# Kernel tuning notes

Hardware: AMD Instinct MI355X
Metric: run time of the kernel (lower is better)

Reference implementation:

```python
import jax, jax.numpy as jnp
import numpy as np

N_HEADS = 16
N_KV_HEADS = 4
HEAD_DIM = 64
ROPE_BASE = 10000.0

def _rope_cos_sin(T, dtype):
    # flash-attn style: cos/sin of shape [T, head_dim//2]
    inv_freq = 1.0 / (ROPE_BASE ** (jnp.arange(0, HEAD_DIM, 2, dtype=jnp.float32) / HEAD_DIM))
    freqs = jnp.arange(T, dtype=jnp.float32)[:, None] * inv_freq[None, :]  # [T, D/2]
    return jnp.cos(freqs).astype(dtype), jnp.sin(freqs).astype(dtype)

def _apply_rope(x, cos, sin):
    # x: [B, H, T, D], non-interleaved rotate-half on full head dim
    d2 = HEAD_DIM // 2
    x1, x2 = x[..., :d2], x[..., d2:]
    c = cos[None, None, :, :]
    s = sin[None, None, :, :]
    return jnp.concatenate([x1 * c - x2 * s, x2 * c + x1 * s], axis=-1)

def setup_inputs() -> dict:
    key = jax.random.key(0)
    ks = jax.random.split(key, 6)
    B, T, D = 1, 4096, 1024
    def g(k, shape, scale):
        return jax.random.normal(k, shape, dtype=jnp.float32) * scale
    return {
        "query": g(ks[0], (B, T, D), 1.0),
        "Wq": g(ks[1], (D, D), D ** -0.5),
        "Wk": g(ks[2], (D, N_KV_HEADS * HEAD_DIM), D ** -0.5),
        "Wv": g(ks[3], (D, N_KV_HEADS * HEAD_DIM), D ** -0.5),
        "W1": g(ks[4], (D, 4 * D), D ** -0.5),
        "W2": g(ks[5], (4 * D, D), (4 * D) ** -0.5),
    }

def reference(query, Wq, Wk, Wv, W1, W2):
    B, T, D = query.shape
    # QKV projections -> [B, H, T, Dh]
    q = (query @ Wq).reshape(B, T, N_HEADS, HEAD_DIM).transpose(0, 2, 1, 3)
    k = (query @ Wk).reshape(B, T, N_KV_HEADS, HEAD_DIM).transpose(0, 2, 1, 3)
    v = (query @ Wv).reshape(B, T, N_KV_HEADS, HEAD_DIM).transpose(0, 2, 1, 3)
    # RoPE (seqlen_offset = 0, no cache)
    cos, sin = _rope_cos_sin(T, q.dtype)
    q = _apply_rope(q, cos, sin)
    k = _apply_rope(k, cos, sin)
    # GQA: repeat KV heads to match Q heads
    n_rep = N_HEADS // N_KV_HEADS
    k = jnp.repeat(k, n_rep, axis=1)
    v = jnp.repeat(v, n_rep, axis=1)
    # Scaled dot-product attention, causal
    scale = HEAD_DIM ** -0.5
    scores = jnp.einsum("bhqd,bhkd->bhqk", q, k) * scale
    i = jnp.arange(T)[:, None]
    j = jnp.arange(T)[None, :]
    scores = jnp.where(j > i, jnp.finfo(scores.dtype).min, scores)
    attn = jax.nn.softmax(scores, axis=-1)
    out = jnp.einsum("bhqk,bhkd->bhqd", attn, v)  # [B, H, T, Dh]
    out = out.transpose(0, 2, 1, 3).reshape(B, T, D)
    # out_proj: Linear -> SiLU -> Linear (use_swiglu=True path)
    return jax.nn.silu(out @ W1) @ W2
```

## Files before the change

kernel.cpp:

```cpp
#include <hip/hip_runtime.h>
#include <stdint.h>

typedef unsigned short u16;
typedef __bf16 bf16x8 __attribute__((ext_vector_type(8)));
typedef float f32x4 __attribute__((ext_vector_type(4)));

#define T_SEQ 4096
#define DMODEL 1024

__device__ __forceinline__ float bf2f(u16 x) {
  union { uint32_t u; float f; } v; v.u = ((uint32_t)x) << 16; return v.f;
}
__device__ __forceinline__ u16 f2bf(float f) {
  union { float f; uint32_t u; } v; v.f = f;
  return (u16)((v.u + 0x7FFFu + ((v.u >> 16) & 1u)) >> 16);
}
__device__ __forceinline__ float fexp2(float x) {
#if __has_builtin(__builtin_amdgcn_exp2f)
  return __builtin_amdgcn_exp2f(x);
#else
  return __expf(x * 0.6931471805599453f);
#endif
}
__device__ __forceinline__ uint32_t pack_bf16(float lo, float hi) {
#if __has_builtin(__builtin_amdgcn_cvt_pk_bf16_f32)
  typedef __bf16 bf16x2_t __attribute__((ext_vector_type(2)));
  union { bf16x2_t v; uint32_t u; } c;
  c.v = __builtin_amdgcn_cvt_pk_bf16_f32(lo, hi);
  return c.u;
#else
  union { float f; uint32_t u; } a, b;
  a.f = lo; b.f = hi;
  return __builtin_amdgcn_perm(b.u + 0x8000u, a.u + 0x8000u, 0x07060302u);
#endif
}
__device__ __forceinline__ void async16(void* lds, const void* g) {
  __builtin_amdgcn_global_load_lds(
      (__attribute__((address_space(1))) void*)const_cast<void*>(g),
      (__attribute__((address_space(3))) void*)lds, 16, 0, 0);
}
__device__ __forceinline__ void storeC(u16* C, size_t i, float v) { C[i] = f2bf(v); }
__device__ __forceinline__ void storeC(float* C, size_t i, float v) { C[i] = v; }

__global__ void __launch_bounds__(256) f2b_copy(const float* __restrict__ in,
                                                u16* __restrict__ out, int n) {
  int idx = (blockIdx.x * 256 + threadIdx.x) * 4;
  if (idx >= n) return;
  float4 v = *(const float4*)(in + idx);
  union { u16 s[4]; uint2 q; } b;
  b.s[0] = f2bf(v.x); b.s[1] = f2bf(v.y); b.s[2] = f2bf(v.z); b.s[3] = f2bf(v.w);
  *(uint2*)(out + idx) = b.q;
}

__global__ void __launch_bounds__(256) wtrans(const float* __restrict__ in,
                                              u16* __restrict__ out, int K, int N) {
  __shared__ float tile[64][65];
  const int n0 = blockIdx.x * 64, k0 = blockIdx.y * 64;
  const int tid = threadIdx.x;
  const int r = tid >> 2, c = (tid & 3) * 16;
#pragma unroll
  for (int j = 0; j < 4; ++j) {
    float4 v = *(const float4*)&in[(size_t)(k0 + r) * N + n0 + c + j * 4];
    tile[r][c + j * 4 + 0] = v.x; tile[r][c + j * 4 + 1] = v.y;
    tile[r][c + j * 4 + 2] = v.z; tile[r][c + j * 4 + 3] = v.w;
  }
  __syncthreads();
  union { u16 s[16]; uint4 q[2]; } buf;
#pragma unroll
  for (int j = 0; j < 16; ++j) buf.s[j] = f2bf(tile[c + j][r]);
  u16* dst = out + (size_t)(n0 + r) * K + k0 + c;
  *(uint4*)(dst) = buf.q[0];
  *(uint4*)(dst + 8) = buf.q[1];
}

__global__ void __launch_bounds__(256) vtrans(const u16* __restrict__ qkv,
                                              u16* __restrict__ Vt) {
  __shared__ u16 tile[64][65];
  const int t0 = blockIdx.x * 64, h = blockIdx.y;
  const int tid = threadIdx.x;
  const int r = tid >> 2, q4 = (tid & 3) * 16;
  const u16* src = qkv + (size_t)(t0 + r) * 1536 + 1280 + h * 64 + q4;
  union { u16 s[16]; uint4 q[2]; } buf;
  buf.q[0] = *(const uint4*)(src);
  buf.q[1] = *(const uint4*)(src + 8);
#pragma unroll
  for (int j = 0; j < 16; ++j) tile[r][q4 + j] = buf.s[j];
  __syncthreads();
#pragma unroll
  for (int j = 0; j < 16; ++j) buf.s[j] = tile[q4 + j][r];
  u16* dst = Vt + ((size_t)h * 64 + r) * T_SEQ + t0 + q4;
  *(uint4*)(dst) = buf.q[0];
  *(uint4*)(dst + 8) = buf.q[1];
}

__global__ void __launch_bounds__(256) rope_qk(const u16* __restrict__ qkv,
                                               u16* __restrict__ Q, u16* __restrict__ Ko) {
  const int t = blockIdx.x;
  const int tid = threadIdx.x;
  const int i = tid & 31;
  const float ang = (float)t * powf(10000.f, -(float)i * (1.f / 32.f));
  float s, c;
  sincosf(ang, &s, &c);
  const u16* row = qkv + (size_t)t * 1536;
  const float QS = 0.125f * 1.4426950408889634f;
  const float cq = c * QS, sq = s * QS;
#pragma unroll
  for (int it = 0; it < 2; ++it) {
    int h = (tid >> 5) + it * 8;
    float x1 = bf2f(row[h * 64 + i]);
    float x2 = bf2f(row[h * 64 + 32 + i]);
    size_t o = ((size_t)h * T_SEQ + t) * 64 + i;
    Q[o] = f2bf(x1 * cq - x2 * sq);
    Q[o + 32] = f2bf(x2 * cq + x1 * sq);
  }
  if (tid < 128) {
    int h = tid >> 5;
    float x1 = bf2f(row[1024 + h * 64 + i]);
    float x2 = bf2f(row[1024 + h * 64 + 32 + i]);
    size_t o = ((size_t)h * T_SEQ + t) * 64 + i;
    Ko[o] = f2bf(x1 * c - x2 * s);
    Ko[o + 32] = f2bf(x2 * c + x1 * s);
  }
}

template <int AM, int ACT, typename OutT>
__global__ void __launch_bounds__(256) gemm_bt(const u16* __restrict__ A,
                                               const u16* __restrict__ Bt,
                                               OutT* __restrict__ C,
                                               int M, int N, int K) {
  __shared__ u16 sA[AM * 32][64];
  __shared__ u16 sB[128][64];
  const int tid = threadIdx.x;
  const int w = tid >> 6, lane = tid & 63;
  const int g = lane >> 4, l15 = lane & 15;
  const int r8 = lane >> 3, c8 = lane & 7;
  const int bm = blockIdx.y * (AM * 32), bn = blockIdx.x * 128;

  f32x4 acc[AM][4];
#pragma unroll
  for (int i = 0; i < AM; ++i)
#pragma unroll
    for (int j = 0; j < 4; ++j) acc[i][j] = (f32x4){0.f, 0.f, 0.f, 0.f};

  const u16* Ag = A + (size_t)(bm + w * (AM * 8) + r8) * K + (c8 ^ r8) * 8;
  const u16* Bg = Bt + (size_t)(bn + w * 32 + r8) * K + (c8 ^ r8) * 8;
  const int mrow = (w >> 1) * (AM * 16), ncol = (w & 1) * 64;
  const int swz = l15 & 7;

  for (int k0 = 0; k0 < K; k0 += 64) {
#pragma unroll
    for (int t = 0; t < AM; ++t)
      async16(&sA[w * (AM * 8) + t * 8][0], Ag + (size_t)(t * 8) * K + k0);
#pragma unroll
    for (int t = 0; t < 4; ++t)
      async16(&sB[w * 32 + t * 8][0], Bg + (size_t)(t * 8) * K + k0);
    __syncthreads();
#pragma unroll
    for (int kk = 0; kk < 2; ++kk) {
      const int cb = ((kk * 4 + g) ^ swz) * 8;
      bf16x8 a[AM], b[4];
#pragma unroll
      for (int i = 0; i < AM; ++i) a[i] = *(const bf16x8*)&sA[mrow + i * 16 + l15][cb];
#pragma unroll
      for (int i = 0; i < 4; ++i) b[i] = *(const bf16x8*)&sB[ncol + i * 16 + l15][cb];
#pragma unroll
      for (int mi = 0; mi < AM; ++mi)
#pragma unroll
        for (int ni = 0; ni < 4; ++ni)
          acc[mi][ni] = __builtin_amdgcn_mfma_f32_16x16x32_bf16(a[mi], b[ni], acc[mi][ni], 0, 0, 0);
    }
    __syncthreads();
  }
#pragma unroll
  for (int mi = 0; mi < AM; ++mi)
#pragma unroll
    for (int ni = 0; ni < 4; ++ni)
#pragma unroll
      for (int r = 0; r < 4; ++r) {
        int row = bm + mrow + mi * 16 + g * 4 + r;
        int col = bn + ncol + ni * 16 + l15;
        float v = acc[mi][ni][r];
        if (ACT == 1) v = v / (1.f + __expf(-v));
        storeC(C, (size_t)row * N + col, v);
      }
}

__global__ void __launch_bounds__(256, 1) attn(const u16* __restrict__ Q,
                                               const u16* __restrict__ K,
                                               const u16* __restrict__ Vt,
                                               u16* __restrict__ O) {
  __shared__ u16 sK[2][64][64];
  __shared__ u16 sV[2][64][64];
  __shared__ u16 sP[4][64][64];
  const int pr = blockIdx.x;
  const int h = blockIdx.y;
  const int kvh = h >> 2;
  const int tid = threadIdx.x;
  const int w = tid >> 6, lane = tid & 63;
  const int g = lane >> 4, l15 = lane & 15;
  const int r8 = lane >> 3, c8 = lane & 7;
  const int swz = l15 & 7, d3 = l15 & 3;
  const int t0 = pr, t1 = 31 - pr;

  bf16x8 qf[2][2][2];
  {
    const u16* Qh = Q + (size_t)h * T_SEQ * 64;
#pragma unroll
    for (int half = 0; half < 2; ++half)
#pragma unroll
      for (int mi = 0; mi < 2; ++mi) {
        const int q = (half ? t1 : t0) * 128 + w * 32 + mi * 16 + l15;
#pragma unroll
        for (int kk = 0; kk < 2; ++kk)
          qf[half][mi][kk] = *(const bf16x8*)(Qh + (size_t)q * 64 + (kk * 4 + g) * 8);
      }
  }

  f32x4 oacc[2][2][4];
  f32x4 lacc[2][2];
#pragma unroll
  for (int half = 0; half < 2; ++half)
#pragma unroll
    for (int mi = 0; mi < 2; ++mi) {
      lacc[half][mi] = (f32x4){0.f, 0.f, 0.f, 0.f};
#pragma unroll
      for (int nd = 0; nd < 4; ++nd) oacc[half][mi][nd] = (f32x4){0.f, 0.f, 0.f, 0.f};
    }

  bf16x8 ONES;
  {
    union { u16 s[8]; bf16x8 v; } o;
#pragma unroll
    for (int i = 0; i < 8; ++i) o.s[i] = 0x3F80;
    ONES = o.v;
  }

  const u16* Kg = K + ((size_t)kvh * T_SEQ + w * 16 + r8) * 64 + (c8 ^ r8) * 8;
  const u16* Vg = Vt + ((size_t)kvh * 64 + w * 16 + r8) * T_SEQ + (c8 ^ r8) * 8;

#define STAGE(J, B)                                                     \
  {                                                                     \
    const int kv0_ = (J) * 64;                                          \
    async16(&sK[B][w * 16 + 0][0], Kg + (size_t)kv0_ * 64);             \
    async16(&sK[B][w * 16 + 8][0], Kg + (size_t)(kv0_ + 8) * 64);       \
    async16(&sV[B][w * 16 + 0][0], Vg + kv0_);                          \
    async16(&sV[B][w * 16 + 8][0], Vg + (size_t)8 * T_SEQ + kv0_);      \
  }

#define BODY(B, ACT0, M0, M1, OFF)                                                \
  {                                                                               \
    const int b_ = (B);                                                           \
    f32x4 s1[2][4], s0[2][4];                                                     \
    _Pragma("unroll") for (int mi = 0; mi < 2; ++mi)                              \
    _Pragma("unroll") for (int kt = 0; kt < 4; ++kt) {                            \
      s1[mi][kt] = (f32x4){0.f, 0.f, 0.f, 0.f};                                   \
      if (ACT0) s0[mi][kt] = (f32x4){0.f, 0.f, 0.f, 0.f};                         \
    }                                                                             \
    _Pragma("unroll") for (int kt = 0; kt < 4; ++kt)                              \
    _Pragma("unroll") for (int kk = 0; kk < 2; ++kk) {                            \
      bf16x8 kf = *(const bf16x8*)&sK[b_][kt * 16 + l15][((kk * 4 + g) ^ swz) * 8]; \
      _Pragma("unroll") for (int mi = 0; mi < 2; ++mi) {                          \
        s1[mi][kt] = __builtin_amdgcn_mfma_f32_16x16x32_bf16(kf, qf[1][mi][kk], s1[mi][kt], 0, 0, 0); \
        if (ACT0)                                                                 \
          s0[mi][kt] = __builtin_amdgcn_mfma_f32_16x16x32_bf16(kf, qf[0][mi][kk], s0[mi][kt], 0, 0, 0); \
      }                                                                           \
    }                                                                             \
    _Pragma("unroll") for (int mi = 0; mi < 2; ++mi) {                            \
      const int thr_ = w * 32 + mi * 16 + l15 - (OFF);                            \
      _Pragma("unroll") for (int kt = 0; kt < 4; ++kt) {                          \
        float p_[4];                                                              \
        _Pragma("unroll") for (int r = 0; r < 4; ++r) {                           \
          float p = fexp2(s1[mi][kt][r]);                                         \
          if (M1 && (kt * 16 + g * 4 + r > thr_)) p = 0.f;                        \
          p_[r] = p;                                                              \
        }                                                                         \
        uint2 pk;                                                                 \
        pk.x = pack_bf16(p_[0], p_[1]);                                           \
        pk.y = pack_bf16(p_[2], p_[3]);                                           \
        *(uint2*)&sP[w][32 + mi * 16 + l15][(kt ^ d3) * 16 + g * 4] = pk;         \
      }                                                                           \
      if (ACT0) {                                                                 \
        _Pragma("unroll") for (int kt = 0; kt < 4; ++kt) {                        \
          float p_[4];                                                            \
          _Pragma("unroll") for (int r = 0; r < 4; ++r) {                         \
            float p = fexp2(s0[mi][kt][r]);                                       \
            if (M0 && (kt * 16 + g * 4 + r > thr_)) p = 0.f;                      \
            p_[r] = p;                                                            \
          }                                                                       \
          uint2 pk;                                                               \
          pk.x = pack_bf16(p_[0], p_[1]);                                         \
          pk.y = pack_bf16(p_[2], p_[3]);                                         \
          *(uint2*)&sP[w][mi * 16 + l15][(kt ^ d3) * 16 + g * 4] = pk;            \
        }                                                                         \
      }                                                                           \
    }                                                                             \
    __builtin_amdgcn_wave_barrier();          \
    _Pragma("unroll") for (int kk = 0; kk < 2; ++kk) {                            \
      const int pb_ = (((kk * 2 + (g >> 1)) ^ d3) * 16 + (g & 1) * 8);            \
      bf16x8 pf1[2], pf0[2];                                                      \
      _Pragma("unroll") for (int mi = 0; mi < 2; ++mi) {                          \
        pf1[mi] = *(const bf16x8*)&sP[w][32 + mi * 16 + l15][pb_];                \
        if (ACT0) pf0[mi] = *(const bf16x8*)&sP[w][mi * 16 + l15][pb_];           \
      }                                                                           \
      _Pragma("unroll") for (int mi = 0; mi < 2; ++mi) {                          \
        lacc[1][mi] = __builtin_amdgcn_mfma_f32_16x16x32_bf16(pf1[mi], ONES, lacc[1][mi], 0, 0, 0); \
        if (ACT0)                                                                 \
          lacc[0][mi] = __builtin_amdgcn_mfma_f32_16x16x32_bf16(pf0[mi], ONES, lacc[0][mi], 0, 0, 0); \
      }                                                                           \
      _Pragma("unroll") for (int nd = 0; nd < 4; ++nd) {                          \
        bf16x8 vf = *(const bf16x8*)&sV[b_][nd * 16 + l15][((kk * 4 + g) ^ swz) * 8]; \
        _Pragma("unroll") for (int mi = 0; mi < 2; ++mi) {                        \
          oacc[1][mi][nd] = __builtin_amdgcn_mfma_f32_16x16x32_bf16(pf1[mi], vf, oacc[1][mi][nd], 0, 0, 0); \
          if (ACT0)                                                               \
            oacc[0][mi][nd] = __builtin_amdgcn_mfma_f32_16x16x32_bf16(pf0[mi], vf, oacc[0][mi][nd], 0, 0, 0); \
        }                                                                         \
      }                                                                           \
    }                                                                             \
  }

  STAGE(0, 0);
  int j = 0;
  for (; j < 2 * t0; ++j) {
    __syncthreads();
    STAGE(j + 1, (j + 1) & 1);
    BODY(j & 1, true, false, false, 0);
  }
  {
    __syncthreads();
    STAGE(j + 1, (j + 1) & 1);
    BODY(j & 1, true, true, false, 0);
    ++j;
  }
  {
    __syncthreads();
    STAGE(j + 1, (j + 1) & 1);
    BODY(j & 1, true, true, false, 64);
    ++j;
  }
  for (; j < 2 * t1; ++j) {
    __syncthreads();
    STAGE(j + 1, (j + 1) & 1);
    BODY(j & 1, false, false, false, 0);
  }
  {
    __syncthreads();
    STAGE(j + 1, (j + 1) & 1);
    BODY(j & 1, false, false, true, 0);
    ++j;
  }
  {
    __syncthreads();
    BODY(j & 1, false, false, true, 64);
  }
#undef STAGE
#undef BODY

#pragma unroll
  for (int half = 0; half < 2; ++half) {
    const int tb = (half ? t1 : t0) * 128;
#pragma unroll
    for (int mi = 0; mi < 2; ++mi)
#pragma unroll
      for (int r = 0; r < 4; ++r) {
        const float inv = 1.f / lacc[half][mi][r];
        const int trow = tb + w * 32 + mi * 16 + g * 4 + r;
#pragma unroll
        for (int nd = 0; nd < 4; ++nd)
          O[(size_t)trow * DMODEL + h * 64 + nd * 16 + l15] = f2bf(oacc[half][mi][nd][r] * inv);
      }
  }
}

extern "C" void kernel_launch(void* const* d_in, const int* in_sizes, int n_in,
                              void* d_out, int out_size, void* d_ws, size_t ws_size,
                              hipStream_t stream) {
  const float* query = (const float*)d_in[0];
  const float* Wq = (const float*)d_in[1];
  const float* Wk = (const float*)d_in[2];
  const float* Wv = (const float*)d_in[3];
  const float* W1 = (const float*)d_in[4];
  const float* W2 = (const float*)d_in[5];
  float* out = (float*)d_out;

  char* ws = (char*)d_ws;
  size_t off = 0;
  auto alloc = [&](size_t bytes) { char* p = ws + off; off += (bytes + 255) & ~(size_t)255; return p; };
  u16* Xb   = (u16*)alloc((size_t)4096 * 1024 * 2);
  u16* QKVb = (u16*)alloc((size_t)4096 * 1536 * 2);
  u16* Qb   = (u16*)alloc((size_t)16 * 4096 * 64 * 2);
  u16* Kb   = (u16*)alloc((size_t)4 * 4096 * 64 * 2);
  u16* Vtb  = (u16*)alloc((size_t)4 * 4096 * 64 * 2);
  u16* H    = (u16*)ws;
  u16* WqkvT = (u16*)alloc((size_t)1536 * 1024 * 2);
  u16* W1T   = (u16*)alloc((size_t)4096 * 1024 * 2);
  u16* W2T   = (u16*)alloc((size_t)1024 * 4096 * 2);
  u16* AO    = (u16*)alloc((size_t)4096 * 1024 * 2);
  (void)ws_size; (void)in_sizes; (void)n_in; (void)out_size;

  f2b_copy<<<4096, 256, 0, stream>>>(query, Xb, 4096 * 1024);
  wtrans<<<dim3(16, 16), 256, 0, stream>>>(Wq, WqkvT, 1024, 1024);
  wtrans<<<dim3(4, 16), 256, 0, stream>>>(Wk, WqkvT + (size_t)1024 * 1024, 1024, 256);
  wtrans<<<dim3(4, 16), 256, 0, stream>>>(Wv, WqkvT + (size_t)1280 * 1024, 1024, 256);
  wtrans<<<dim3(64, 16), 256, 0, stream>>>(W1, W1T, 1024, 4096);
  wtrans<<<dim3(16, 64), 256, 0, stream>>>(W2, W2T, 4096, 1024);

  gemm_bt<2, 0, u16><<<dim3(12, 64), 256, 0, stream>>>(Xb, WqkvT, QKVb, 4096, 1536, 1024);
  rope_qk<<<4096, 256, 0, stream>>>(QKVb, Qb, Kb);
  vtrans<<<dim3(64, 4), 256, 0, stream>>>(QKVb, Vtb);
  attn<<<dim3(16, 16), 256, 0, stream>>>(Qb, Kb, Vtb, AO);
  gemm_bt<4, 1, u16><<<dim3(32, 32), 256, 0, stream>>>(AO, W1T, H, 4096, 4096, 1024);
  gemm_bt<2, 0, float><<<dim3(8, 64), 256, 0, stream>>>(H, W2T, out, 4096, 1024, 4096);
}
```

Baseline: 344.5 us.

## Split attention KV loop across two blocks with a combine kernel

Each attention block's key/value tile range is split into even and odd tiles, handled by two separate blocks. This doubles the grid to 512 blocks and lets two blocks share a CU via launch_bounds(256,2). Each split writes unnormalised bf16 partial outputs and row sums into reused workspace, and a new combine kernel adds the partials and normalises them. The P shared-memory swizzle is replaced with row padding (68 columns). The intent is better occupancy and CU utilisation at the cost of an extra kernel, extra global traffic, and a bf16 rounding of the partials before they are combined.

```diff
diff --git a/kernel.cpp b/kernel.cpp
--- a/kernel.cpp
+++ b/kernel.cpp
@@ -185,22 +185,30 @@
       }
 }
 
-__global__ void __launch_bounds__(256, 1) attn(const u16* __restrict__ Q,
+__global__ void __launch_bounds__(256, 2) attn(const u16* __restrict__ Q,
                                                const u16* __restrict__ K,
                                                const u16* __restrict__ Vt,
-                                               u16* __restrict__ O) {
+                                               u16* __restrict__ O0,
+                                               u16* __restrict__ O1,
+                                               float* __restrict__ L0,
+                                               float* __restrict__ L1) {
   __shared__ u16 sK[2][64][64];
   __shared__ u16 sV[2][64][64];
-  __shared__ u16 sP[4][64][64];
-  const int pr = blockIdx.x;
+  __shared__ u16 sP[4][64][68];
+  const int pr = blockIdx.x >> 1;
+  const int split = blockIdx.x & 1;
   const int h = blockIdx.y;
   const int kvh = h >> 2;
   const int tid = threadIdx.x;
   const int w = tid >> 6, lane = tid & 63;
   const int g = lane >> 4, l15 = lane & 15;
   const int r8 = lane >> 3, c8 = lane & 7;
-  const int swz = l15 & 7, d3 = l15 & 3;
+  const int swz = l15 & 7;
   const int t0 = pr, t1 = 31 - pr;
+  const int off = split * 64;
+
+  u16* Op = split ? O1 : O0;
+  float* Lp = split ? L1 : L0;
 
   bf16x8 qf[2][2][2];
   {
@@ -247,7 +255,7 @@
     async16(&sV[B][w * 16 + 8][0], Vg + (size_t)8 * T_SEQ + kv0_);      \
   }
 
-#define BODY(B, ACT0, M0, M1, OFF)                                                \
+#define BODY(B, ACT0, M0, M1)                                                     \
   {                                                                               \
     const int b_ = (B);                                                           \
     f32x4 s1[2][4], s0[2][4];                                                     \
@@ -266,7 +274,7 @@
       }                                                                           \
     }                                                                             \
     _Pragma("unroll") for (int mi = 0; mi < 2; ++mi) {                            \
-      const int thr_ = w * 32 + mi * 16 + l15 - (OFF);                            \
+      const int thr_ = w * 32 + mi * 16 + l15 - off;                              \
       _Pragma("unroll") for (int kt = 0; kt < 4; ++kt) {                          \
         float p_[4];                                                              \
         _Pragma("unroll") for (int r = 0; r < 4; ++r) {                           \
@@ -277,7 +285,7 @@
         uint2 pk;                                                                 \
         pk.x = pack_bf16(p_[0], p_[1]);                                           \
         pk.y = pack_bf16(p_[2], p_[3]);                                           \
-        *(uint2*)&sP[w][32 + mi * 16 + l15][(kt ^ d3) * 16 + g * 4] = pk;         \
+        *(uint2*)&sP[w][32 + mi * 16 + l15][kt * 16 + g * 4] = pk;                \
       }                                                                           \
       if (ACT0) {                                                                 \
         _Pragma("unroll") for (int kt = 0; kt < 4; ++kt) {                        \
@@ -290,17 +298,16 @@
           uint2 pk;                                                               \
           pk.x = pack_bf16(p_[0], p_[1]);                                         \
           pk.y = pack_bf16(p_[2], p_[3]);                                         \
-          *(uint2*)&sP[w][mi * 16 + l15][(kt ^ d3) * 16 + g * 4] = pk;            \
+          *(uint2*)&sP[w][mi * 16 + l15][kt * 16 + g * 4] = pk;                   \
         }                                                                         \
       }                                                                           \
     }                                                                             \
     __builtin_amdgcn_wave_barrier();          \
     _Pragma("unroll") for (int kk = 0; kk < 2; ++kk) {                            \
-      const int pb_ = (((kk * 2 + (g >> 1)) ^ d3) * 16 + (g & 1) * 8);            \
       bf16x8 pf1[2], pf0[2];                                                      \
       _Pragma("unroll") for (int mi = 0; mi < 2; ++mi) {                          \
-        pf1[mi] = *(const bf16x8*)&sP[w][32 + mi * 16 + l15][pb_];                \
-        if (ACT0) pf0[mi] = *(const bf16x8*)&sP[w][mi * 16 + l15][pb_];           \
+        pf1[mi] = *(const bf16x8*)&sP[w][32 + mi * 16 + l15][kk * 32 + g * 8];    \
+        if (ACT0) pf0[mi] = *(const bf16x8*)&sP[w][mi * 16 + l15][kk * 32 + g * 8]; \
       }                                                                           \
       _Pragma("unroll") for (int mi = 0; mi < 2; ++mi) {                          \
         lacc[1][mi] = __builtin_amdgcn_mfma_f32_16x16x32_bf16(pf1[mi], ONES, lacc[1][mi], 0, 0, 0); \
@@ -318,39 +325,28 @@
     }                                                                             \
   }
 
-  STAGE(0, 0);
-  int j = 0;
-  for (; j < 2 * t0; ++j) {
-    __syncthreads();
-    STAGE(j + 1, (j + 1) & 1);
-    BODY(j & 1, true, false, false, 0);
+  const int e0 = 2 * t0 + split, e1 = 2 * t1 + split;
+  STAGE(split, 0);
+  int jj = split, b = 0;
+  for (; jj < e0; jj += 2, b ^= 1) {
+    __syncthreads();
+    STAGE(jj + 2, b ^ 1);
+    BODY(b, true, false, false);
   }
   {
     __syncthreads();
-    STAGE(j + 1, (j + 1) & 1);
-    BODY(j & 1, true, true, false, 0);
-    ++j;
+    STAGE(jj + 2, b ^ 1);
+    BODY(b, true, true, false);
+    jj += 2; b ^= 1;
+  }
+  for (; jj < e1; jj += 2, b ^= 1) {
+    __syncthreads();
+    STAGE(jj + 2, b ^ 1);
+    BODY(b, false, false, false);
   }
   {
     __syncthreads();
-    STAGE(j + 1, (j + 1) & 1);
-    BODY(j & 1, true, true, false, 64);
-    ++j;
-  }
-  for (; j < 2 * t1; ++j) {
-    __syncthreads();
-    STAGE(j + 1, (j + 1) & 1);
-    BODY(j & 1, false, false, false, 0);
-  }
-  {
-    __syncthreads();
-    STAGE(j + 1, (j + 1) & 1);
-    BODY(j & 1, false, false, true, 0);
-    ++j;
-  }
-  {
-    __syncthreads();
-    BODY(j & 1, false, false, true, 64);
+    BODY(b, false, false, true);
   }
 #undef STAGE
 #undef BODY
@@ -362,13 +358,30 @@
     for (int mi = 0; mi < 2; ++mi)
 #pragma unroll
       for (int r = 0; r < 4; ++r) {
-        const float inv = 1.f / lacc[half][mi][r];
         const int trow = tb + w * 32 + mi * 16 + g * 4 + r;
 #pragma unroll
         for (int nd = 0; nd < 4; ++nd)
-          O[(size_t)trow * DMODEL + h * 64 + nd * 16 + l15] = f2bf(oacc[half][mi][nd][r] * inv);
+          Op[(size_t)trow * DMODEL + h * 64 + nd * 16 + l15] = f2bf(oacc[half][mi][nd][r]);
+        if (l15 == 0) Lp[h * T_SEQ + trow] = lacc[half][mi][r];
       }
   }
+}
+
+__global__ void __launch_bounds__(256) attn_combine(const u16* __restrict__ O0,
+                                                    const u16* __restrict__ O1,
+                                                    const float* __restrict__ L0,
+                                                    const float* __restrict__ L1,
+                                                    u16* __restrict__ AO) {
+  const int t = blockIdx.x, tid = threadIdx.x;
+  const int h = tid >> 4, d4 = (tid & 15) * 4;
+  const float inv = 1.f / (L0[h * T_SEQ + t] + L1[h * T_SEQ + t]);
+  const size_t idx = (size_t)t * DMODEL + h * 64 + d4;
+  union { uint2 q; u16 s[4]; } a, b, o;
+  a.q = *(const uint2*)(O0 + idx);
+  b.q = *(const uint2*)(O1 + idx);
+#pragma unroll
+  for (int i = 0; i < 4; ++i) o.s[i] = f2bf((bf2f(a.s[i]) + bf2f(b.s[i])) * inv);
+  *(uint2*)(AO + idx) = o.q;
 }
 
 extern "C" void kernel_launch(void* const* d_in, const int* in_sizes, int n_in,
@@ -391,6 +404,10 @@
   u16* Kb   = (u16*)alloc((size_t)4 * 4096 * 64 * 2);
   u16* Vtb  = (u16*)alloc((size_t)4 * 4096 * 64 * 2);
   u16* H    = (u16*)ws;
+  u16*   O0p = Xb;
+  u16*   O1p = QKVb;
+  float* L0p = (float*)(QKVb + (size_t)4096 * 1024);
+  float* L1p = L0p + 16 * T_SEQ;
   u16* WqkvT = (u16*)alloc((size_t)1536 * 1024 * 2);
   u16* W1T   = (u16*)alloc((size_t)4096 * 1024 * 2);
   u16* W2T   = (u16*)alloc((size_t)1024 * 4096 * 2);
@@ -407,7 +424,8 @@
   gemm_bt<2, 0, u16><<<dim3(12, 64), 256, 0, stream>>>(Xb, WqkvT, QKVb, 4096, 1536, 1024);
   rope_qk<<<4096, 256, 0, stream>>>(QKVb, Qb, Kb);
   vtrans<<<dim3(64, 4), 256, 0, stream>>>(QKVb, Vtb);
-  attn<<<dim3(16, 16), 256, 0, stream>>>(Qb, Kb, Vtb, AO);
+  attn<<<dim3(32, 16), 256, 0, stream>>>(Qb, Kb, Vtb, O0p, O1p, L0p, L1p);
+  attn_combine<<<4096, 256, 0, stream>>>(O0p, O1p, L0p, L1p, AO);
   gemm_bt<4, 1, u16><<<dim3(32, 32), 256, 0, stream>>>(AO, W1T, H, 4096, 4096, 1024);
   gemm_bt<2, 0, float><<<dim3(8, 64), 256, 0, stream>>>(H, W2T, out, 4096, 1024, 4096);
 }
```

Measured after the change: 318.0 us. -7.7%, faster.
